# Kernel optimization log

Measured on AMD Instinct MI355X. Metric: run time of the kernel, lower is better.

Reference implementation:

```python
import jax, jax.numpy as jnp
import numpy as np

B, S, D_MODEL = 2, 8192, 768
NUM_HEADS = 12
R = 4          # dilation_rate (= number of independent attention branches)
SEG = 512      # segment_size


def setup_inputs() -> dict:
    key = jax.random.key(0)
    ks = jax.random.split(key, 3)
    x = jax.random.normal(ks[0], (B, S, D_MODEL), jnp.float32)
    # Per-offset MHA weights: fused qkv proj and output proj (bias zeros)
    Wqkv = jax.random.normal(ks[1], (R, 3 * D_MODEL, D_MODEL), jnp.float32) * 0.02
    bqkv = jnp.zeros((R, 3 * D_MODEL), jnp.float32)
    Wout = jax.random.normal(ks[2], (R, D_MODEL, D_MODEL), jnp.float32) * 0.02
    bout = jnp.zeros((R, D_MODEL), jnp.float32)
    return {"x": x, "Wqkv": Wqkv, "bqkv": bqkv, "Wout": Wout, "bout": bout,
            "num_heads": NUM_HEADS}


def reference(x, Wqkv, bqkv, Wout, bout, num_heads):
    Bb, Ss, D = x.shape
    r = Wqkv.shape[0]
    L = Ss // r                # tokens per dilation offset
    n_seg = L // SEG           # segments per offset
    hd = D // num_heads

    # Dilated strided gather: x[:, o::r, :] for all offsets o -> (r, B, L, D)
    xo = jnp.moveaxis(x.reshape(Bb, L, r, D), 2, 0)

    # Per-offset fused qkv projection
    qkv = jnp.einsum('rbld,red->rble', xo, Wqkv) + bqkv[:, None, None, :]
    q, k, v = jnp.split(qkv, 3, axis=-1)
    seg = lambda t: t.reshape(r, Bb, n_seg, SEG, num_heads, hd)
    q, k, v = seg(q), seg(k), seg(v)  # (r, B, n_seg, SEG, H, hd)

    scale = 1.0 / np.sqrt(hd).astype(np.float32)
    scores = jnp.einsum('rbnqhd,rbnkhd->rbnhqk', q, k) * scale
    attn = jax.nn.softmax(scores, axis=-1)
    ctx = jnp.einsum('rbnhqk,rbnkhd->rbnqhd', attn, v).reshape(r, Bb, L, D)

    # Per-offset output projection
    out = jnp.einsum('rbld,red->rble', ctx, Wout) + bout[:, None, None, :]  # (r,B,L,D)

    # Scatter each offset's output back to its strided positions, zeros elsewhere,
    # then concat over offsets along the feature dim -> (B, S, r*D)
    res = jnp.zeros((Bb, Ss, r * D), x.dtype)
    for o in range(r):  # fixed small loop over dilation offsets
        res = res.at[:, o::r, o * D:(o + 1) * D].set(out[o])
    return res
```

## Files before the change

### kernel.cpp

```cpp
#include <hip/hip_runtime.h>

constexpr int Bb   = 2;
constexpr int S    = 8192;
constexpr int D    = 768;
constexpr int H    = 12;
constexpr int HD   = 64;
constexpr int R    = 4;
constexpr int L    = 2048;
constexpr int SEG  = 512;
constexpr int NSEG = 4;
constexpr int E3   = 3 * D;
constexpr int RD   = R * D;

typedef _Float16 f16x8 __attribute__((ext_vector_type(8)));
typedef _Float16 f16x4 __attribute__((ext_vector_type(4)));
typedef float    f32x4 __attribute__((ext_vector_type(4)));

#define AS1 __attribute__((address_space(1)))
#define AS3 __attribute__((address_space(3)))

__device__ __forceinline__ void gld16(const void* g, void* l) {
    __builtin_amdgcn_global_load_lds((AS1 void*)g, (AS3 void*)l, 16, 0, 0);
}

__global__ __launch_bounds__(256) void zero_fill(float4* __restrict__ p, int n4)
{
    int i = blockIdx.x * 256 + threadIdx.x;
    const int stride = gridDim.x * 256;
    float4 z; z.x = z.y = z.z = z.w = 0.f;
    for (; i < n4; i += stride) p[i] = z;
}

__global__ __launch_bounds__(256) void conv_one(const float4* __restrict__ x,
                                                f16x4* __restrict__ o, int n4)
{
    int i = blockIdx.x * 256 + threadIdx.x;
    const int stride = gridDim.x * 256;
    for (; i < n4; i += stride) {
        float4 v = x[i];
        f16x4 h;
        h[0] = (_Float16)v.x; h[1] = (_Float16)v.y;
        h[2] = (_Float16)v.z; h[3] = (_Float16)v.w;
        o[i] = h;
    }
}

template <int MODE>
__global__ __launch_bounds__(256) void mfma_gemm(const _Float16* __restrict__ Ah0,
                                                 const _Float16* __restrict__ Wh0,
                                                 const float* __restrict__ B0,
                                                 _Float16* __restrict__ Q0,
                                                 _Float16* __restrict__ K0,
                                                 _Float16* __restrict__ V0,
                                                 float* __restrict__ C0)
{
    const int z = blockIdx.z;
    const int r = z >> 1, b = z & 1;

    const _Float16* Ah; const _Float16* Wh; const float* bias;
    int lda;
    if (MODE == 0) {
        Ah = Ah0 + ((size_t)b * S + r) * D;  lda = RD;
        Wh = Wh0 + (size_t)r * E3 * D;
        bias = B0 + r * E3;
    } else {
        Ah = Ah0 + (size_t)z * L * D;        lda = D;
        Wh = Wh0 + (size_t)r * D * D;
        bias = B0 + r * D;
    }

    const int tid  = threadIdx.x;
    const int wave = tid >> 6;
    const int lane = tid & 63;
    const int lw   = lane & 15;
    const int quad = lane >> 4;
    const int wm   = wave & 1, wn = wave >> 1;
    const int m0 = blockIdx.y * 128, n0 = blockIdx.x * 128;

    __shared__ _Float16 sm[2][2][4096];

    f32x4 acc[4][4];
    #pragma unroll
    for (int mt = 0; mt < 4; mt++)
        #pragma unroll
        for (int nt = 0; nt < 4; nt++)
            acc[mt][nt] = f32x4{0.f, 0.f, 0.f, 0.f};

    const int srow = lane & 15;
    const int scol = (lane >> 4) * 8;

    auto stage = [&](int buf, int k0) {
        #pragma unroll
        for (int i = 0; i < 4; i++) {
            const int idx  = wave * 4 + i;
            const int tile = idx >> 3, g = idx & 7;
            const _Float16* src = (tile == 0) ? Ah : Wh;
            const int ldr   = (tile == 0) ? lda : D;
            const int base0 = (tile == 0) ? m0 : n0;
            gld16(src + (size_t)(base0 + g * 16 + srow) * ldr + k0 + scol,
                  &sm[buf][tile][g * 512]);
        }
    };

    stage(0, 0);

    for (int k = 0; k < 24; k++) {
        __syncthreads();
        const int buf = k & 1;
        f16x8 af[4], bf[4];
        #pragma unroll
        for (int mt = 0; mt < 4; mt++)
            af[mt] = *(const f16x8*)&sm[buf][0][(wm * 4 + mt) * 512 + quad * 128 + lw * 8];
        #pragma unroll
        for (int nt = 0; nt < 4; nt++)
            bf[nt] = *(const f16x8*)&sm[buf][1][(wn * 4 + nt) * 512 + quad * 128 + lw * 8];
        if (k + 1 < 24) stage(buf ^ 1, (k + 1) * 32);
        #pragma unroll
        for (int mt = 0; mt < 4; mt++)
            #pragma unroll
            for (int nt = 0; nt < 4; nt++)
                acc[mt][nt] = __builtin_amdgcn_mfma_f32_16x16x32_f16(af[mt], bf[nt], acc[mt][nt], 0, 0, 0);
    }
    __syncthreads();

    float bv[4];
    #pragma unroll
    for (int nt = 0; nt < 4; nt++)
        bv[nt] = bias[n0 + wn * 64 + nt * 16 + lw];

    if (MODE == 0) {
        const int reg = n0 / D;
        if (reg < 2) {
            _Float16* G = (reg == 0 ? Q0 : K0) + (size_t)z * L * D;
            const int colbase = (n0 - reg * D) + wn * 64;
            _Float16* wbuf = &sm[0][0][wave * 2048];
            #pragma unroll
            for (int p = 0; p < 2; p++) {
                #pragma unroll
                for (int mtl = 0; mtl < 2; mtl++) {
                    const int mt = p * 2 + mtl;
                    #pragma unroll
                    for (int nt = 0; nt < 4; nt++)
                        #pragma unroll
                        for (int rr = 0; rr < 4; rr++)
                            wbuf[(mtl * 16 + quad * 4 + rr) * 64 + nt * 16 + lw] =
                                (_Float16)(acc[mt][nt][rr] + bv[nt]);
                }
                asm volatile("s_waitcnt lgkmcnt(0)" ::: "memory");
                #pragma unroll
                for (int j = 0; j < 4; j++) {
                    const int rl = (lane >> 3) + j * 8;
                    f16x8 v = *(const f16x8*)&wbuf[rl * 64 + (lane & 7) * 8];
                    const int l = m0 + wm * 64 + p * 32 + rl;
                    *(f16x8*)(G + (size_t)l * D + colbase + (lane & 7) * 8) = v;
                }
                asm volatile("s_waitcnt lgkmcnt(0)" ::: "memory");
            }
        } else {
            #pragma unroll
            for (int nt = 0; nt < 4; nt++) {
                const int e  = (n0 - 2 * D) + wn * 64 + nt * 16 + lw;
                const int hh = e >> 6, hd = e & 63;
                #pragma unroll
                for (int mt = 0; mt < 4; mt++) {
                    const int l = m0 + wm * 64 + mt * 16 + quad * 4;
                    const int ns = l >> 9, key = l & 511;
                    f16x4 v;
                    #pragma unroll
                    for (int rr = 0; rr < 4; rr++)
                        v[rr] = (_Float16)(acc[mt][nt][rr] + bv[nt]);
                    *(f16x4*)(V0 + ((size_t)((z * H + hh) * NSEG + ns)) * (HD * SEG)
                              + (size_t)hd * SEG + key) = v;
                }
            }
        }
    } else {
        float* Cb = C0 + (size_t)b * S * RD + r * RD + r * D;
        #pragma unroll
        for (int mt = 0; mt < 4; mt++)
            #pragma unroll
            for (int nt = 0; nt < 4; nt++) {
                const int col = n0 + wn * 64 + nt * 16 + lw;
                #pragma unroll
                for (int rr = 0; rr < 4; rr++)
                    Cb[(size_t)(m0 + wm * 64 + mt * 16 + quad * 4 + rr) * (R * RD) + col] =
                        acc[mt][nt][rr] + bv[nt];
            }
    }
}

__global__ __launch_bounds__(256) void attn_mfma(const _Float16* __restrict__ Qh,
                                                 const _Float16* __restrict__ Kh,
                                                 const _Float16* __restrict__ Vt,
                                                 _Float16* __restrict__ ctx)
{
    __shared__ _Float16 Ks[4096];
    __shared__ _Float16 Vs[4096];
    __shared__ _Float16 Pw[16384];

    int t = blockIdx.x;
    const int qh = t & 1; t >>= 1;
    const int h  = t % H; t /= H;
    const int n  = t & 3; t >>= 2;
    const int z  = t;

    const int tid  = threadIdx.x;
    const int wave = tid >> 6;
    const int lane = tid & 63;
    const int lw   = lane & 15;
    const int quad = lane >> 4;
    const int srow = lane & 15;
    const int scol = (lane >> 4) * 8;

    const _Float16* Qg = Qh + ((size_t)(z * L + n * SEG + qh * 256)) * D + h * HD;
    #pragma unroll
    for (int i = 0; i < 8; i++) {
        const int qg = wave * 4 + (i >> 1), h2 = i & 1;
        gld16(Qg + (size_t)(qg * 16 + srow) * D + h2 * 32 + scol,
              &Pw[qg * 1024 + h2 * 512]);
    }
    __syncthreads();

    f16x8 qf[4][2];
    #pragma unroll
    for (int mt = 0; mt < 4; mt++)
        #pragma unroll
        for (int kk = 0; kk < 2; kk++)
            qf[mt][kk] = *(const f16x8*)&Pw[(wave * 4 + mt) * 1024 + (kk * 4 + quad) * 128 + lw * 8];

    const _Float16* Kg = Kh + ((size_t)(z * L + n * SEG)) * D + h * HD;
    const _Float16* Vg = Vt + ((size_t)((z * H + h) * NSEG + n)) * (HD * SEG);
    _Float16* Pv = Pw + wave * 4096;

    f32x4 cacc[4][4];
    #pragma unroll
    for (int mt = 0; mt < 4; mt++)
        #pragma unroll
        for (int nt = 0; nt < 4; nt++)
            cacc[mt][nt] = f32x4{0.f, 0.f, 0.f, 0.f};
    float psum[4] = {0.f, 0.f, 0.f, 0.f};

    for (int kt = 0; kt < 8; kt++) {
        __syncthreads();
        #pragma unroll
        for (int i = 0; i < 4; i++) {
            const int idx = wave * 4 + i;
            const int j = idx & 7, g = j >> 1, h2 = j & 1;
            if (idx < 8)
                gld16(Kg + (size_t)(kt * 64 + g * 16 + srow) * D + h2 * 32 + scol,
                      &Ks[g * 1024 + h2 * 512]);
            else
                gld16(Vg + (size_t)(g * 16 + srow) * SEG + kt * 64 + h2 * 32 + scol,
                      &Vs[g * 1024 + h2 * 512]);
        }
        __syncthreads();

        f32x4 Sc[4][4];
        #pragma unroll
        for (int mt = 0; mt < 4; mt++)
            #pragma unroll
            for (int nt = 0; nt < 4; nt++)
                Sc[mt][nt] = f32x4{0.f, 0.f, 0.f, 0.f};
        #pragma unroll
        for (int kk = 0; kk < 2; kk++)
            #pragma unroll
            for (int nt = 0; nt < 4; nt++) {
                f16x8 kf = *(const f16x8*)&Ks[nt * 1024 + (kk * 4 + quad) * 128 + lw * 8];
                #pragma unroll
                for (int mt = 0; mt < 4; mt++)
                    Sc[mt][nt] = __builtin_amdgcn_mfma_f32_16x16x32_f16(kf, qf[mt][kk], Sc[mt][nt], 0, 0, 0);
            }

        #pragma unroll
        for (int mt = 0; mt < 4; mt++)
            #pragma unroll
            for (int nt = 0; nt < 4; nt++) {
                f16x4 p4;
                #pragma unroll
                for (int rr = 0; rr < 4; rr++)
                    p4[rr] = (_Float16)__expf(Sc[mt][nt][rr] * 0.125f);
                *(f16x4*)&Pv[mt * 1024 + (nt * 2 + (quad >> 1)) * 128 + lw * 8 + (quad & 1) * 4] = p4;
            }
        asm volatile("s_waitcnt lgkmcnt(0)" ::: "memory");

        #pragma unroll
        for (int kk = 0; kk < 2; kk++) {
            f16x8 pf[4], vf[4];
            #pragma unroll
            for (int mt = 0; mt < 4; mt++) {
                pf[mt] = *(const f16x8*)&Pv[mt * 1024 + (kk * 4 + quad) * 128 + lw * 8];
                float s = 0.f;
                #pragma unroll
                for (int j = 0; j < 8; j++) s += (float)pf[mt][j];
                psum[mt] += s;
            }
            #pragma unroll
            for (int nt = 0; nt < 4; nt++)
                vf[nt] = *(const f16x8*)&Vs[nt * 1024 + (kk * 4 + quad) * 128 + lw * 8];
            #pragma unroll
            for (int mt = 0; mt < 4; mt++)
                #pragma unroll
                for (int nt = 0; nt < 4; nt++)
                    cacc[mt][nt] = __builtin_amdgcn_mfma_f32_16x16x32_f16(pf[mt], vf[nt], cacc[mt][nt], 0, 0, 0);
        }
    }

    #pragma unroll
    for (int mt = 0; mt < 4; mt++) {
        psum[mt] += __shfl_xor(psum[mt], 16);
        psum[mt] += __shfl_xor(psum[mt], 32);
    }
    _Float16* Cg = ctx + ((size_t)(z * L + n * SEG + qh * 256 + wave * 64)) * D + h * HD;
    #pragma unroll
    for (int mt = 0; mt < 4; mt++)
        #pragma unroll
        for (int rr = 0; rr < 4; rr++) {
            float iv = 1.0f / __shfl(psum[mt], quad * 4 + rr);
            int q = mt * 16 + quad * 4 + rr;
            #pragma unroll
            for (int nt = 0; nt < 4; nt++)
                Cg[(size_t)q * D + nt * 16 + lw] = (_Float16)(cacc[mt][nt][rr] * iv);
        }
}

extern "C" void kernel_launch(void* const* d_in, const int* in_sizes, int n_in,
                              void* d_out, int out_size, void* d_ws, size_t ws_size,
                              hipStream_t stream)
{
    const float* x    = (const float*)d_in[0];
    const float* Wqkv = (const float*)d_in[1];
    const float* bqkv = (const float*)d_in[2];
    const float* Wout = (const float*)d_in[3];
    const float* bout = (const float*)d_in[4];

    float* out = (float*)d_out;

    constexpr size_t NX   = (size_t)Bb * S * D;
    constexpr size_t NWQ  = (size_t)R * E3 * D;
    constexpr size_t NWO  = (size_t)R * D * D;
    constexpr size_t NTOK = (size_t)R * Bb * L;

    _Float16* Xh  = (_Float16*)d_ws;
    _Float16* Wqh = Xh  + NX;
    _Float16* Wo  = Wqh + NWQ;
    _Float16* Qh  = Wo  + NWO;
    _Float16* Kh  = Qh  + NTOK * D;
    _Float16* Vt  = Kh  + NTOK * D;
    _Float16* ctx = Vt  + NTOK * D;

    zero_fill<<<2048, 256, 0, stream>>>((float4*)out, (Bb * S * RD) / 4);

    conv_one<<<2048, 256, 0, stream>>>((const float4*)x, (f16x4*)Xh, (int)(NX / 4));
    conv_one<<<2048, 256, 0, stream>>>((const float4*)Wqkv, (f16x4*)Wqh, (int)(NWQ / 4));
    conv_one<<<1024, 256, 0, stream>>>((const float4*)Wout, (f16x4*)Wo, (int)(NWO / 4));

    mfma_gemm<0><<<dim3(E3 / 128, L / 128, R * Bb), 256, 0, stream>>>(
        Xh, Wqh, bqkv, Qh, Kh, Vt, nullptr);

    attn_mfma<<<R * Bb * NSEG * H * 2, 256, 0, stream>>>(Qh, Kh, Vt, ctx);

    mfma_gemm<1><<<dim3(D / 128, L / 128, R * Bb), 256, 0, stream>>>(
        ctx, Wo, bout, nullptr, nullptr, nullptr, out);
}
```

Measured before the change: 488.3 us.

## Triple-buffer GEMM and attention loads, fuse zero-fill into output GEMM, remap blocks

Both the projection GEMMs and the attention kernel move from double to triple buffering. They issue loads two stages ahead and wait with explicit vmcnt/lgkmcnt counters plus a raw s_barrier instead of two __syncthreads per iteration. The separate zero_fill kernel is removed; the output GEMM now writes zeros to the other offsets' column blocks of each row alongside the real values. Block indices are remapped across the 8 XCDs for locality. Together these remove a full pass over the output and expose more load/compute overlap, at the cost of more LDS and hand-tuned wait counts.

```diff
diff --git a/kernel.cpp b/kernel.cpp
--- a/kernel.cpp
+++ b/kernel.cpp
@@ -23,14 +23,6 @@
     __builtin_amdgcn_global_load_lds((AS1 void*)g, (AS3 void*)l, 16, 0, 0);
 }
 
-__global__ __launch_bounds__(256) void zero_fill(float4* __restrict__ p, int n4)
-{
-    int i = blockIdx.x * 256 + threadIdx.x;
-    const int stride = gridDim.x * 256;
-    float4 z; z.x = z.y = z.z = z.w = 0.f;
-    for (; i < n4; i += stride) p[i] = z;
-}
-
 __global__ __launch_bounds__(256) void conv_one(const float4* __restrict__ x,
                                                 f16x4* __restrict__ o, int n4)
 {
@@ -54,7 +46,12 @@
                                                  _Float16* __restrict__ V0,
                                                  float* __restrict__ C0)
 {
-    const int z = blockIdx.z;
+    constexpr int NXB = (MODE == 0) ? 18 : 6;
+    constexpr int NWG = NXB * 16 * 8;
+    const int wg = ((int)blockIdx.x & 7) * (NWG >> 3) + ((int)blockIdx.x >> 3);
+    const int n0 = (wg % NXB) * 128;
+    const int m0 = ((wg / NXB) & 15) * 128;
+    const int z  = wg / (NXB * 16);
     const int r = z >> 1, b = z & 1;
 
     const _Float16* Ah; const _Float16* Wh; const float* bias;
@@ -75,9 +72,8 @@
     const int lw   = lane & 15;
     const int quad = lane >> 4;
     const int wm   = wave & 1, wn = wave >> 1;
-    const int m0 = blockIdx.y * 128, n0 = blockIdx.x * 128;
-
-    __shared__ _Float16 sm[2][2][4096];
+
+    __shared__ _Float16 sm[3][2][4096];
 
     f32x4 acc[4][4];
     #pragma unroll
@@ -103,10 +99,16 @@
     };
 
     stage(0, 0);
+    stage(1, 32);
 
     for (int k = 0; k < 24; k++) {
-        __syncthreads();
-        const int buf = k & 1;
+        asm volatile("s_waitcnt lgkmcnt(0)" ::: "memory");
+        if (k == 23) asm volatile("s_waitcnt vmcnt(0)" ::: "memory");
+        else         asm volatile("s_waitcnt vmcnt(4)" ::: "memory");
+        __builtin_amdgcn_s_barrier();
+        __builtin_amdgcn_sched_barrier(0);
+
+        const int buf = k % 3;
         f16x8 af[4], bf[4];
         #pragma unroll
         for (int mt = 0; mt < 4; mt++)
@@ -114,7 +116,7 @@
         #pragma unroll
         for (int nt = 0; nt < 4; nt++)
             bf[nt] = *(const f16x8*)&sm[buf][1][(wn * 4 + nt) * 512 + quad * 128 + lw * 8];
-        if (k + 1 < 24) stage(buf ^ 1, (k + 1) * 32);
+        if (k + 2 < 24) stage((k + 2) % 3, (k + 2) * 32);
         #pragma unroll
         for (int mt = 0; mt < 4; mt++)
             #pragma unroll
@@ -175,16 +177,21 @@
             }
         }
     } else {
-        float* Cb = C0 + (size_t)b * S * RD + r * RD + r * D;
+        float* Crow = C0 + (size_t)b * S * RD;
         #pragma unroll
         for (int mt = 0; mt < 4; mt++)
             #pragma unroll
             for (int nt = 0; nt < 4; nt++) {
                 const int col = n0 + wn * 64 + nt * 16 + lw;
                 #pragma unroll
-                for (int rr = 0; rr < 4; rr++)
-                    Cb[(size_t)(m0 + wm * 64 + mt * 16 + quad * 4 + rr) * (R * RD) + col] =
-                        acc[mt][nt][rr] + bv[nt];
+                for (int rr = 0; rr < 4; rr++) {
+                    const int l = m0 + wm * 64 + mt * 16 + quad * 4 + rr;
+                    const float val = acc[mt][nt][rr] + bv[nt];
+                    const size_t rowoff = (size_t)(l * R + r) * RD;
+                    #pragma unroll
+                    for (int rp = 0; rp < 4; rp++)
+                        Crow[rowoff + rp * D + col] = (rp == r) ? val : 0.f;
+                }
             }
     }
 }
@@ -194,11 +201,11 @@
                                                  const _Float16* __restrict__ Vt,
                                                  _Float16* __restrict__ ctx)
 {
-    __shared__ _Float16 Ks[4096];
-    __shared__ _Float16 Vs[4096];
+    __shared__ _Float16 Ks[3][4096];
+    __shared__ _Float16 Vs[3][4096];
     __shared__ _Float16 Pw[16384];
 
-    int t = blockIdx.x;
+    int t = ((int)blockIdx.x & 7) * 96 + ((int)blockIdx.x >> 3);
     const int qh = t & 1; t >>= 1;
     const int h  = t % H; t /= H;
     const int n  = t & 3; t >>= 2;
@@ -232,28 +239,40 @@
     const _Float16* Vg = Vt + ((size_t)((z * H + h) * NSEG + n)) * (HD * SEG);
     _Float16* Pv = Pw + wave * 4096;
 
-    f32x4 cacc[4][4];
-    #pragma unroll
-    for (int mt = 0; mt < 4; mt++)
-        #pragma unroll
-        for (int nt = 0; nt < 4; nt++)
-            cacc[mt][nt] = f32x4{0.f, 0.f, 0.f, 0.f};
-    float psum[4] = {0.f, 0.f, 0.f, 0.f};
-
-    for (int kt = 0; kt < 8; kt++) {
-        __syncthreads();
+    auto stageKV = [&](int buf, int kt) {
         #pragma unroll
         for (int i = 0; i < 4; i++) {
             const int idx = wave * 4 + i;
             const int j = idx & 7, g = j >> 1, h2 = j & 1;
             if (idx < 8)
                 gld16(Kg + (size_t)(kt * 64 + g * 16 + srow) * D + h2 * 32 + scol,
-                      &Ks[g * 1024 + h2 * 512]);
+                      &Ks[buf][g * 1024 + h2 * 512]);
             else
                 gld16(Vg + (size_t)(g * 16 + srow) * SEG + kt * 64 + h2 * 32 + scol,
-                      &Vs[g * 1024 + h2 * 512]);
-        }
-        __syncthreads();
+                      &Vs[buf][g * 1024 + h2 * 512]);
+        }
+    };
+
+    f32x4 cacc[4][4];
+    #pragma unroll
+    for (int mt = 0; mt < 4; mt++)
+        #pragma unroll
+        for (int nt = 0; nt < 4; nt++)
+            cacc[mt][nt] = f32x4{0.f, 0.f, 0.f, 0.f};
+    float psum[4] = {0.f, 0.f, 0.f, 0.f};
+
+    stageKV(0, 0);
+    stageKV(1, 1);
+
+    for (int kt = 0; kt < 8; kt++) {
+        asm volatile("s_waitcnt lgkmcnt(0)" ::: "memory");
+        if (kt == 7) asm volatile("s_waitcnt vmcnt(0)" ::: "memory");
+        else         asm volatile("s_waitcnt vmcnt(4)" ::: "memory");
+        __builtin_amdgcn_s_barrier();
+        __builtin_amdgcn_sched_barrier(0);
+
+        const int buf = kt % 3;
+        if (kt + 2 < 8) stageKV((kt + 2) % 3, kt + 2);
 
         f32x4 Sc[4][4];
         #pragma unroll
@@ -265,7 +284,7 @@
         for (int kk = 0; kk < 2; kk++)
             #pragma unroll
             for (int nt = 0; nt < 4; nt++) {
-                f16x8 kf = *(const f16x8*)&Ks[nt * 1024 + (kk * 4 + quad) * 128 + lw * 8];
+                f16x8 kf = *(const f16x8*)&Ks[buf][nt * 1024 + (kk * 4 + quad) * 128 + lw * 8];
                 #pragma unroll
                 for (int mt = 0; mt < 4; mt++)
                     Sc[mt][nt] = __builtin_amdgcn_mfma_f32_16x16x32_f16(kf, qf[mt][kk], Sc[mt][nt], 0, 0, 0);
@@ -296,7 +315,7 @@
             }
             #pragma unroll
             for (int nt = 0; nt < 4; nt++)
-                vf[nt] = *(const f16x8*)&Vs[nt * 1024 + (kk * 4 + quad) * 128 + lw * 8];
+                vf[nt] = *(const f16x8*)&Vs[buf][nt * 1024 + (kk * 4 + quad) * 128 + lw * 8];
             #pragma unroll
             for (int mt = 0; mt < 4; mt++)
                 #pragma unroll
@@ -348,17 +367,15 @@
     _Float16* Vt  = Kh  + NTOK * D;
     _Float16* ctx = Vt  + NTOK * D;
 
-    zero_fill<<<2048, 256, 0, stream>>>((float4*)out, (Bb * S * RD) / 4);
-
     conv_one<<<2048, 256, 0, stream>>>((const float4*)x, (f16x4*)Xh, (int)(NX / 4));
     conv_one<<<2048, 256, 0, stream>>>((const float4*)Wqkv, (f16x4*)Wqh, (int)(NWQ / 4));
     conv_one<<<1024, 256, 0, stream>>>((const float4*)Wout, (f16x4*)Wo, (int)(NWO / 4));
 
-    mfma_gemm<0><<<dim3(E3 / 128, L / 128, R * Bb), 256, 0, stream>>>(
+    mfma_gemm<0><<<E3 / 128 * (L / 128) * R * Bb, 256, 0, stream>>>(
         Xh, Wqh, bqkv, Qh, Kh, Vt, nullptr);
 
     attn_mfma<<<R * Bb * NSEG * H * 2, 256, 0, stream>>>(Qh, Kh, Vt, ctx);
 
-    mfma_gemm<1><<<dim3(D / 128, L / 128, R * Bb), 256, 0, stream>>>(
+    mfma_gemm<1><<<D / 128 * (L / 128) * R * Bb, 256, 0, stream>>>(
         ctx, Wo, bout, nullptr, nullptr, nullptr, out);
 }
```

Result: faster. 465.6 us (-4.6%).
